# Performance work log

Hardware: AMD Instinct MI355X
Metric: run time of the kernel (lower is better)

The kernel has to match this reference:

```python
import jax, jax.numpy as jnp
import numpy as np

B, L, D_IN = 4, 2048, 80
D, H, DFF, WIN = 128, 16, 128, 64
DH = D // H
BN_EPS = 1e-5


def sinusoidal_positional_encoding(l, d, dtype):
    # Faithful to source: pos_j = 10000 ** (j / d) (exponent j/d, not 2j/d)
    n = d // 2 + (d % 2 == 1)
    pos_i = jnp.arange(l, dtype=dtype)[:, None]                  # [L,1]
    pos_j = jnp.power(jnp.asarray(10000.0, dtype), jnp.arange(n, dtype=dtype) / d)  # [n]
    ang = pos_i / pos_j                                          # [L,n]
    pos = jnp.stack([jnp.sin(ang), jnp.cos(ang)], axis=-1).reshape(l, -1)
    return pos[:, :d]                                            # [L,D]


def local_window_disallowed_mask(l, win):
    # Source: mask starts as ones (True = disallowed), zeros only strictly
    i = jnp.arange(l)
    diff = jnp.abs(i[:, None] - i[None, :])
    allowed = (diff >= 1) & (diff <= win)
    return ~allowed                                              # [L,L] bool, True = masked


def setup_inputs() -> dict:
    key = jax.random.key(0)
    ks = jax.random.split(key, 17)
    s = 0.05  # weight scale for numerical stability
    return {
        "x": jax.random.normal(ks[0], (B, L, D_IN), jnp.float32),
        "conv_w": jax.random.normal(ks[1], (D, D_IN), jnp.float32) * s,
        "conv_b": jax.random.normal(ks[2], (D,), jnp.float32) * s,
        "bn_g": jax.random.uniform(ks[3], (D,), jnp.float32, 0.5, 1.5),
        "bn_b": jax.random.normal(ks[4], (D,), jnp.float32) * s,
        "bn_rm": jax.random.normal(ks[5], (D,), jnp.float32) * s,
        "bn_rv": jax.random.uniform(ks[6], (D,), jnp.float32, 0.5, 1.5),
        "in_proj_w": jax.random.normal(ks[7], (3 * D, D), jnp.float32) * s,
        "in_proj_b": jax.random.normal(ks[8], (3 * D,), jnp.float32) * s,
        "out_w": jax.random.normal(ks[9], (D, D), jnp.float32) * s,
        "out_b": jax.random.normal(ks[10], (D,), jnp.float32) * s,
        "ff_w1": jax.random.normal(ks[11], (DFF, D), jnp.float32) * s,
        "ff_b1": jax.random.normal(ks[12], (DFF,), jnp.float32) * s,
        "ff_w2": jax.random.normal(ks[13], (D, DFF), jnp.float32) * s,
        "ff_b2": jax.random.normal(ks[14], (D,), jnp.float32) * s,
        "fc_w": jax.random.normal(ks[15], (D_IN, D), jnp.float32) * s,
        "fc_b": jax.random.normal(ks[16], (D_IN,), jnp.float32) * s,
    }


def _forward(x, conv_w, conv_b, bn_g, bn_b, bn_rm, bn_rv,
             in_proj_w, in_proj_b, out_w, out_b,
             ff_w1, ff_b1, ff_w2, ff_b2, fc_w, fc_b):
    b, l, _ = x.shape
    dt = x.dtype
    # Conv1d(kernel=1) + ReLU + BatchNorm1d (eval mode, running stats)
    h = jax.nn.relu(jnp.einsum('bli,oi->blo', x, conv_w) + conv_b)     # [B,L,D]
    h = (h - bn_rm) * (bn_g * jax.lax.rsqrt(bn_rv + BN_EPS)) + bn_b
    # positional encoding
    h = h + sinusoidal_positional_encoding(l, D, dt)
    # MultiheadAttention (torch semantics: joint in_proj, scaled dot, out_proj)
    qkv = jnp.einsum('bld,ed->ble', h, in_proj_w) + in_proj_b          # [B,L,3D]
    q, k, v = jnp.split(qkv, 3, axis=-1)
    q = q.reshape(b, l, H, DH).transpose(0, 2, 1, 3)                   # [B,H,L,dh]
    k = k.reshape(b, l, H, DH).transpose(0, 2, 1, 3)
    v = v.reshape(b, l, H, DH).transpose(0, 2, 1, 3)
    scores = jnp.einsum('bhqd,bhkd->bhqk', q, k) / jnp.sqrt(jnp.asarray(DH, dt))
    mask = local_window_disallowed_mask(l, WIN)                        # True = masked
    scores = jnp.where(mask, jnp.finfo(dt).min, scores)
    attn = jax.nn.softmax(scores, axis=-1)                             # [B,H,L,L]
    ctx = jnp.einsum('bhqk,bhkd->bhqd', attn, v)
    ctx = ctx.transpose(0, 2, 1, 3).reshape(b, l, D)
    attn_out = jnp.einsum('bld,od->blo', ctx, out_w) + out_b           # [B,L,D]
    # FFN (no residual in source)
    f = jax.nn.relu(jnp.einsum('bld,fd->blf', attn_out, ff_w1) + ff_b1)
    f = jnp.einsum('blf,df->bld', f, ff_w2) + ff_b2                    # [B,L,D]
    # final head
    return jnp.einsum('bld,od->blo', f, fc_w) + fc_b                   # [B,L,80]


def reference(x, conv_w, conv_b, bn_g, bn_b, bn_rm, bn_rv,
              in_proj_w, in_proj_b, out_w, out_b,
              ff_w1, ff_b1, ff_w2, ff_b2, fc_w, fc_b):
    return _forward(x, conv_w, conv_b, bn_g, bn_b, bn_rm, bn_rv,
                    in_proj_w, in_proj_b, out_w, out_b,
                    ff_w1, ff_b1, ff_w2, ff_b2, fc_w, fc_b)
```

## Files before the change

### kernel.cpp

```cpp
#include <hip/hip_runtime.h>
#include <hip/hip_bf16.h>
#include <math.h>

constexpr int B_ = 4, L_ = 2048, DIN = 80, D_ = 128, H_ = 16, DH = 8;
constexpr int T_ = B_ * L_;
constexpr int LDX = T_;
constexpr int BHL = B_ * H_ * L_;

__device__ float g_xT  [DIN * T_];
__device__ float g_posT[D_ * L_];
__device__ float g_h   [D_ * T_];
__device__ float g_qkv [3 * D_ * T_];
__device__ float g_ctx [D_ * T_];
__device__ float g_f1  [D_ * T_];
__device__ float g_pA  [2 * 8 * BHL];
__device__ float g_pl  [2 * BHL];
__device__ float g_WconvT[DIN * D_];
__device__ float g_WqkvT [D_ * 3 * D_];
__device__ float g_Wf1T  [D_ * D_];
__device__ float g_WfcT  [D_ * D_];
__device__ float g_bf1   [D_];
__device__ float g_bfc   [D_];

__global__ __launch_bounds__(256) void prep_kernel(
        const float* __restrict__ x,
        const float* __restrict__ conv_w,
        const float* __restrict__ in_proj_w,
        const float* __restrict__ out_w,  const float* __restrict__ out_b,
        const float* __restrict__ ff_w1,  const float* __restrict__ ff_b1,
        const float* __restrict__ ff_w2,  const float* __restrict__ ff_b2,
        const float* __restrict__ fc_w,   const float* __restrict__ fc_b) {
    __shared__ float smem[80 * 65];
    int bid = blockIdx.x, tid = threadIdx.x;

    if (bid < 128) {
        int t0 = bid * 64;
        for (int i = tid; i < 64 * 80; i += 256) {
            int t = i / 80, k = i - t * 80;
            smem[k * 65 + t] = x[(size_t)(t0) * 80 + i];
        }
        __syncthreads();
        for (int i = tid; i < 80 * 64; i += 256) {
            int k = i >> 6, tt = i & 63;
            g_xT[(size_t)k * T_ + t0 + tt] = smem[k * 65 + tt];
        }
        return;
    }
    if (bid < 640) {
        int idx = (bid - 128) * 256 + tid;
        int l = idx >> 6, j = idx & 63;
        float inv = __expf((float)j * (-9.210340371976184f / 128.0f));
        float ang = (float)l * inv;
        g_posT[(2 * j) * L_ + l]     = sinf(ang);
        g_posT[(2 * j + 1) * L_ + l] = cosf(ang);
        return;
    }
    if (bid < 680) {
        int e = (bid - 640) * 256 + tid;
        int o = e / 80, k = e - o * 80;
        g_WconvT[k * D_ + o] = conv_w[e];
        return;
    }
    if (bid < 872) {
        int e = (bid - 680) * 256 + tid;
        int o = e >> 7, k = e & 127;
        g_WqkvT[k * (3 * D_) + o] = in_proj_w[e];
        return;
    }
    float* rowbuf = smem;
    float* red = smem + 256;
    if (bid < 936) {
        int sub = tid >> 7, k = tid & 127;
        int f = (bid - 872) * 2 + sub;
        rowbuf[sub * 128 + k] = ff_w1[f * 128 + k];
        __syncthreads();
        float acc = 0.f;
#pragma unroll 8
        for (int o = 0; o < 128; o++)
            acc = fmaf(rowbuf[sub * 128 + o], out_w[o * 128 + k], acc);
        g_Wf1T[k * 128 + f] = acc;
        red[tid] = rowbuf[sub * 128 + k] * out_b[k];
        __syncthreads();
        for (int s = 64; s > 0; s >>= 1) {
            if (k < s) red[tid] += red[tid + s];
            __syncthreads();
        }
        if (k == 0) g_bf1[f] = red[sub * 128] + ff_b1[f];
        return;
    }
    {
        int sub = tid >> 7, k = tid & 127;
        int o = (bid - 936) * 2 + sub;
        rowbuf[sub * 128 + k] = (o < 80) ? fc_w[o * 128 + k] : 0.f;
        __syncthreads();
        float acc = 0.f;
#pragma unroll 8
        for (int d = 0; d < 128; d++)
            acc = fmaf(rowbuf[sub * 128 + d], ff_w2[d * 128 + k], acc);
        g_WfcT[k * 128 + o] = acc;
        red[tid] = rowbuf[sub * 128 + k] * ff_b2[k];
        __syncthreads();
        for (int s = 64; s > 0; s >>= 1) {
            if (k < s) red[tid] += red[tid + s];
            __syncthreads();
        }
        if (k == 0) g_bfc[o] = (o < 80) ? (red[sub * 128] + fc_b[o]) : 0.f;
        return;
    }
}

template <int K, int BK, int BN, int LDW, int EPI>
__global__ __launch_bounds__(256) void gemm_kernel(
        const float* __restrict__ X, const float* __restrict__ Wt,
        const float* __restrict__ bias,
        const float* __restrict__ bg, const float* __restrict__ bb,
        const float* __restrict__ brm, const float* __restrict__ brv,
        float* __restrict__ Y) {
    constexpr int TN = BN / 16;
    __shared__ float Xs[BK][64];
    __shared__ float Ws[BK][BN];
    int tid = threadIdx.x;
    int t0 = blockIdx.x * 64;
    int cb = blockIdx.y * BN;
    int tc = tid & 15, tr = tid >> 4;

    float acc[4][TN] = {};
    for (int kc = 0; kc < K; kc += BK) {
        for (int i = tid; i < BK * 16; i += 256) {
            int k = i >> 4, f = i & 15;
            *(float4*)&Xs[k][f * 4] =
                *(const float4*)&X[(size_t)(kc + k) * LDX + t0 + f * 4];
        }
        for (int i = tid; i < BK * (BN / 4); i += 256) {
            int k = i / (BN / 4), f = i - k * (BN / 4);
            *(float4*)&Ws[k][f * 4] =
                *(const float4*)&Wt[(size_t)(kc + k) * LDW + cb + f * 4];
        }
        __syncthreads();
#pragma unroll 4
        for (int k = 0; k < BK; ++k) {
            float4 a = *(float4*)&Xs[k][tr * 4];
            float av[4] = {a.x, a.y, a.z, a.w};
            float wv[TN];
#pragma unroll
            for (int jj = 0; jj < TN; jj++) wv[jj] = Ws[k][tc * TN + jj];
#pragma unroll
            for (int i = 0; i < 4; i++)
#pragma unroll
                for (int jj = 0; jj < TN; jj++)
                    acc[i][jj] = fmaf(av[i], wv[jj], acc[i][jj]);
        }
        __syncthreads();
    }

    if (EPI == 4) {
#pragma unroll
        for (int jj = 0; jj < TN; jj++) {
            int c = cb + tc * TN + jj;
            if (c < 80) {
                float bv = bias[c];
#pragma unroll
                for (int i = 0; i < 4; i++) {
                    int t = t0 + tr * 4 + i;
                    Y[(size_t)t * 80 + c] = acc[i][jj] + bv;
                }
            }
        }
        return;
    }
#pragma unroll
    for (int jj = 0; jj < TN; jj++) {
        int c = cb + tc * TN + jj;
        float bv = bias[c];
        float vs[4];
#pragma unroll
        for (int i = 0; i < 4; i++) {
            float v = acc[i][jj] + bv;
            if (EPI == 1) v = fmaxf(v, 0.0f);
            if (EPI == 2) {
                v = fmaxf(v, 0.0f);
                v = (v - brm[c]) * (bg[c] * rsqrtf(brv[c] + 1e-5f)) + bb[c];
                v += g_posT[c * L_ + ((t0 & 2047) + tr * 4 + i)];
            }
            vs[i] = v;
        }
        *(float4*)&Y[(size_t)c * LDX + t0 + tr * 4] = *(float4*)vs;
    }
}

__global__ __launch_bounds__(128) void attn_kernel() {
    __shared__ float4 SK[2][2][160];
    __shared__ float4 SV[2][2][160];
    int bh = blockIdx.x, tile = blockIdx.y, hf = blockIdx.z;
    int b = bh >> 4, h = bh & 15;
    int qb = tile * 256;
    int tid = threadIdx.x;
    int jbase = hf ? (qb + 1) : (qb - 64);
    int tb = b * L_;

    for (int c16 = 0; c16 < 16; c16++) {
        int d = (c16 < 8) ? c16 : (c16 - 8);
        int ch = ((c16 < 8) ? 128 : 256) + h * 8 + d;
        const float* src = g_qkv + (size_t)ch * LDX + tb;
        for (int s = tid; s < 319; s += 128) {
            int j = jbase + s;
            float v = ((unsigned)j < (unsigned)L_) ? src[j] : 0.f;
            float4* arr = (c16 < 8) ? &SK[s & 1][d >> 2][s >> 1]
                                    : &SV[s & 1][d >> 2][s >> 1];
            ((float*)arr)[d & 3] = v;
        }
    }
    __syncthreads();

    const float sc = 0.35355339059327373f;
    int q0 = qb + 2 * tid;
    float qa[8], qc[8];
    {
        const float* qsrc = g_qkv + tb;
#pragma unroll
        for (int d = 0; d < 8; d++) {
            qa[d] = qsrc[(size_t)(h * 8 + d) * LDX + q0] * sc;
            qc[d] = qsrc[(size_t)(h * 8 + d) * LDX + q0 + 1] * sc;
        }
    }

    float l0 = 0.f, l1 = 0.f;
    float A0[8] = {}, A1[8] = {};
    int j00 = jbase + 2 * tid;

    auto step = [&](int it, bool m0, bool m1) {
        int p = it & 1, idx = tid + (it >> 1);
        float4 ka = SK[p][0][idx], kb = SK[p][1][idx];
        float kv[8] = {ka.x, ka.y, ka.z, ka.w, kb.x, kb.y, kb.z, kb.w};
        float s0 = 0.f, s1 = 0.f;
#pragma unroll
        for (int d = 0; d < 8; d++) {
            s0 = fmaf(qa[d], kv[d], s0);
            s1 = fmaf(qc[d], kv[d], s1);
        }
        bool jv = (unsigned)(j00 + it) < (unsigned)L_;
        float w0 = (m0 && jv) ? __expf(s0) : 0.f;
        float w1 = (m1 && jv) ? __expf(s1) : 0.f;
        l0 += w0; l1 += w1;
        float4 va = SV[p][0][idx], vb = SV[p][1][idx];
        float vv[8] = {va.x, va.y, va.z, va.w, vb.x, vb.y, vb.z, vb.w};
#pragma unroll
        for (int d = 0; d < 8; d++) {
            A0[d] = fmaf(w0, vv[d], A0[d]);
            A1[d] = fmaf(w1, vv[d], A1[d]);
        }
    };

    step(0, true, false);
#pragma unroll 2
    for (int it = 1; it <= 63; it++) step(it, true, true);
    step(64, false, true);

    int base = bh * L_ + q0;
#pragma unroll
    for (int d = 0; d < 8; d++) {
        g_pA[(hf * 8 + d) * BHL + base]     = A0[d];
        g_pA[(hf * 8 + d) * BHL + base + 1] = A1[d];
    }
    g_pl[hf * BHL + base]     = l0;
    g_pl[hf * BHL + base + 1] = l1;
}

__global__ __launch_bounds__(256) void combine_kernel() {
    int gq = blockIdx.x * 256 + threadIdx.x;
    int bh = gq >> 11, l = gq & 2047;
    int b = bh >> 4, h = bh & 15;
    float ls = g_pl[gq] + g_pl[BHL + gq];
    float inv = 1.f / ls;
#pragma unroll
    for (int d = 0; d < 8; d++) {
        float v = (g_pA[d * BHL + gq] + g_pA[(8 + d) * BHL + gq]) * inv;
        g_ctx[(size_t)(h * 8 + d) * LDX + b * L_ + l] = v;
    }
}

extern "C" void kernel_launch(void* const* d_in, const int* in_sizes, int n_in,
                              void* d_out, int out_size, void* d_ws, size_t ws_size,
                              hipStream_t stream) {
    const float* x         = (const float*)d_in[0];
    const float* conv_w    = (const float*)d_in[1];
    const float* conv_b    = (const float*)d_in[2];
    const float* bn_g      = (const float*)d_in[3];
    const float* bn_b      = (const float*)d_in[4];
    const float* bn_rm     = (const float*)d_in[5];
    const float* bn_rv     = (const float*)d_in[6];
    const float* in_proj_w = (const float*)d_in[7];
    const float* in_proj_b = (const float*)d_in[8];
    const float* out_w     = (const float*)d_in[9];
    const float* out_b     = (const float*)d_in[10];
    const float* ff_w1     = (const float*)d_in[11];
    const float* ff_b1     = (const float*)d_in[12];
    const float* ff_w2     = (const float*)d_in[13];
    const float* ff_b2     = (const float*)d_in[14];
    const float* fc_w      = (const float*)d_in[15];
    const float* fc_b      = (const float*)d_in[16];

    float *p_xT, *p_h, *p_qkv, *p_ctx, *p_f1;
    float *p_WconvT, *p_WqkvT, *p_Wf1T, *p_WfcT, *p_bf1, *p_bfc;
    hipGetSymbolAddress((void**)&p_xT,     HIP_SYMBOL(g_xT));
    hipGetSymbolAddress((void**)&p_h,      HIP_SYMBOL(g_h));
    hipGetSymbolAddress((void**)&p_qkv,    HIP_SYMBOL(g_qkv));
    hipGetSymbolAddress((void**)&p_ctx,    HIP_SYMBOL(g_ctx));
    hipGetSymbolAddress((void**)&p_f1,     HIP_SYMBOL(g_f1));
    hipGetSymbolAddress((void**)&p_WconvT, HIP_SYMBOL(g_WconvT));
    hipGetSymbolAddress((void**)&p_WqkvT,  HIP_SYMBOL(g_WqkvT));
    hipGetSymbolAddress((void**)&p_Wf1T,   HIP_SYMBOL(g_Wf1T));
    hipGetSymbolAddress((void**)&p_WfcT,   HIP_SYMBOL(g_WfcT));
    hipGetSymbolAddress((void**)&p_bf1,    HIP_SYMBOL(g_bf1));
    hipGetSymbolAddress((void**)&p_bfc,    HIP_SYMBOL(g_bfc));

    prep_kernel<<<1000, 256, 0, stream>>>(x, conv_w, in_proj_w, out_w, out_b,
                                          ff_w1, ff_b1, ff_w2, ff_b2, fc_w, fc_b);

    gemm_kernel<80, 80, 32, 128, 2><<<dim3(128, 4), 256, 0, stream>>>(
        p_xT, p_WconvT, conv_b, bn_g, bn_b, bn_rm, bn_rv, p_h);

    gemm_kernel<128, 64, 64, 384, 0><<<dim3(128, 6), 256, 0, stream>>>(
        p_h, p_WqkvT, in_proj_b, nullptr, nullptr, nullptr, nullptr, p_qkv);

    attn_kernel<<<dim3(64, 8, 2), 128, 0, stream>>>();
    combine_kernel<<<512, 256, 0, stream>>>();

    gemm_kernel<128, 128, 32, 128, 1><<<dim3(128, 4), 256, 0, stream>>>(
        p_ctx, p_Wf1T, p_bf1, nullptr, nullptr, nullptr, nullptr, p_f1);

    gemm_kernel<128, 128, 32, 128, 4><<<dim3(128, 3), 256, 0, stream>>>(
        p_f1, p_WfcT, p_bfc, nullptr, nullptr, nullptr, nullptr, (float*)d_out);
}
```

Measured before the change: 164.4 us.

## Merge all stages into one cooperative persistent kernel with grid syncs

```diff
diff --git a/kernel.cpp b/kernel.cpp
--- a/kernel.cpp
+++ b/kernel.cpp
@@ -1,6 +1,8 @@
 #include <hip/hip_runtime.h>
-#include <hip/hip_bf16.h>
+#include <hip/hip_cooperative_groups.h>
 #include <math.h>
+
+namespace cg = cooperative_groups;
 
 constexpr int B_ = 4, L_ = 2048, DIN = 80, D_ = 128, H_ = 16, DH = 8;
 constexpr int T_ = B_ * L_;
@@ -22,192 +24,176 @@
 __device__ float g_bf1   [D_];
 __device__ float g_bfc   [D_];
 
-__global__ __launch_bounds__(256) void prep_kernel(
-        const float* __restrict__ x,
-        const float* __restrict__ conv_w,
-        const float* __restrict__ in_proj_w,
-        const float* __restrict__ out_w,  const float* __restrict__ out_b,
-        const float* __restrict__ ff_w1,  const float* __restrict__ ff_b1,
-        const float* __restrict__ ff_w2,  const float* __restrict__ ff_b2,
-        const float* __restrict__ fc_w,   const float* __restrict__ fc_b) {
-    __shared__ float smem[80 * 65];
-    int bid = blockIdx.x, tid = threadIdx.x;
-
-    if (bid < 128) {
-        int t0 = bid * 64;
+struct Params {
+    const float *x, *conv_w, *conv_b, *bn_g, *bn_b, *bn_rm, *bn_rv;
+    const float *in_proj_w, *in_proj_b, *out_w, *out_b;
+    const float *ff_w1, *ff_b1, *ff_w2, *ff_b2, *fc_w, *fc_b;
+    float* out;
+};
+
+__device__ void prep_unit(int u, int tid, const Params& p, float* smem) {
+    if (u < 128) {
+        int t0 = u * 64;
         for (int i = tid; i < 64 * 80; i += 256) {
             int t = i / 80, k = i - t * 80;
-            smem[k * 65 + t] = x[(size_t)(t0) * 80 + i];
+            smem[k * 65 + t] = p.x[(size_t)t0 * 80 + i];
         }
         __syncthreads();
         for (int i = tid; i < 80 * 64; i += 256) {
             int k = i >> 6, tt = i & 63;
             g_xT[(size_t)k * T_ + t0 + tt] = smem[k * 65 + tt];
         }
-        return;
-    }
-    if (bid < 640) {
-        int idx = (bid - 128) * 256 + tid;
+    } else if (u < 640) {
+        int idx = (u - 128) * 256 + tid;
         int l = idx >> 6, j = idx & 63;
         float inv = __expf((float)j * (-9.210340371976184f / 128.0f));
         float ang = (float)l * inv;
         g_posT[(2 * j) * L_ + l]     = sinf(ang);
         g_posT[(2 * j + 1) * L_ + l] = cosf(ang);
-        return;
-    }
-    if (bid < 680) {
-        int e = (bid - 640) * 256 + tid;
+    } else if (u < 680) {
+        int e = (u - 640) * 256 + tid;
         int o = e / 80, k = e - o * 80;
-        g_WconvT[k * D_ + o] = conv_w[e];
-        return;
-    }
-    if (bid < 872) {
-        int e = (bid - 680) * 256 + tid;
+        g_WconvT[k * D_ + o] = p.conv_w[e];
+    } else if (u < 872) {
+        int e = (u - 680) * 256 + tid;
         int o = e >> 7, k = e & 127;
-        g_WqkvT[k * (3 * D_) + o] = in_proj_w[e];
-        return;
-    }
-    float* rowbuf = smem;
-    float* red = smem + 256;
-    if (bid < 936) {
+        g_WqkvT[k * (3 * D_) + o] = p.in_proj_w[e];
+    } else if (u < 936) {
+        float* rowbuf = smem; float* red = smem + 256;
         int sub = tid >> 7, k = tid & 127;
-        int f = (bid - 872) * 2 + sub;
-        rowbuf[sub * 128 + k] = ff_w1[f * 128 + k];
+        int f = (u - 872) * 2 + sub;
+        rowbuf[sub * 128 + k] = p.ff_w1[f * 128 + k];
         __syncthreads();
         float acc = 0.f;
 #pragma unroll 8
         for (int o = 0; o < 128; o++)
-            acc = fmaf(rowbuf[sub * 128 + o], out_w[o * 128 + k], acc);
+            acc = fmaf(rowbuf[sub * 128 + o], p.out_w[o * 128 + k], acc);
         g_Wf1T[k * 128 + f] = acc;
-        red[tid] = rowbuf[sub * 128 + k] * out_b[k];
+        red[tid] = rowbuf[sub * 128 + k] * p.out_b[k];
         __syncthreads();
         for (int s = 64; s > 0; s >>= 1) {
             if (k < s) red[tid] += red[tid + s];
             __syncthreads();
         }
-        if (k == 0) g_bf1[f] = red[sub * 128] + ff_b1[f];
-        return;
-    }
-    {
+        if (k == 0) g_bf1[f] = red[sub * 128] + p.ff_b1[f];
+    } else {
+        float* rowbuf = smem; float* red = smem + 256;
         int sub = tid >> 7, k = tid & 127;
-        int o = (bid - 936) * 2 + sub;
-        rowbuf[sub * 128 + k] = (o < 80) ? fc_w[o * 128 + k] : 0.f;
+        int o = (u - 936) * 2 + sub;
+        rowbuf[sub * 128 + k] = (o < 80) ? p.fc_w[o * 128 + k] : 0.f;
         __syncthreads();
         float acc = 0.f;
 #pragma unroll 8
         for (int d = 0; d < 128; d++)
-            acc = fmaf(rowbuf[sub * 128 + d], ff_w2[d * 128 + k], acc);
+            acc = fmaf(rowbuf[sub * 128 + d], p.ff_w2[d * 128 + k], acc);
         g_WfcT[k * 128 + o] = acc;
-        red[tid] = rowbuf[sub * 128 + k] * ff_b2[k];
+        red[tid] = rowbuf[sub * 128 + k] * p.ff_b2[k];
         __syncthreads();
         for (int s = 64; s > 0; s >>= 1) {
             if (k < s) red[tid] += red[tid + s];
             __syncthreads();
         }
-        if (k == 0) g_bfc[o] = (o < 80) ? (red[sub * 128] + fc_b[o]) : 0.f;
-        return;
+        if (k == 0) g_bfc[o] = (o < 80) ? (red[sub * 128] + p.fc_b[o]) : 0.f;
     }
 }
 
 template <int K, int BK, int BN, int LDW, int EPI>
-__global__ __launch_bounds__(256) void gemm_kernel(
-        const float* __restrict__ X, const float* __restrict__ Wt,
-        const float* __restrict__ bias,
-        const float* __restrict__ bg, const float* __restrict__ bb,
-        const float* __restrict__ brm, const float* __restrict__ brv,
-        float* __restrict__ Y) {
+__device__ void gemm_tile(float* smem, const float* __restrict__ X,
+                          const float* __restrict__ Wt,
+                          const float* __restrict__ bias,
+                          const float* __restrict__ bg, const float* __restrict__ bb,
+                          const float* __restrict__ brm, const float* __restrict__ brv,
+                          float* __restrict__ Y, int tx, int cy, int tid) {
     constexpr int TN = BN / 16;
-    __shared__ float Xs[BK][64];
-    __shared__ float Ws[BK][BN];
-    int tid = threadIdx.x;
-    int t0 = blockIdx.x * 64;
-    int cb = blockIdx.y * BN;
+    float* Xs = smem;
+    float* Ws = smem + BK * 64;
+    int t0 = tx * 64, cb = cy * BN;
     int tc = tid & 15, tr = tid >> 4;
-
     float acc[4][TN] = {};
     for (int kc = 0; kc < K; kc += BK) {
         for (int i = tid; i < BK * 16; i += 256) {
             int k = i >> 4, f = i & 15;
-            *(float4*)&Xs[k][f * 4] =
+            *(float4*)&Xs[k * 64 + f * 4] =
                 *(const float4*)&X[(size_t)(kc + k) * LDX + t0 + f * 4];
         }
         for (int i = tid; i < BK * (BN / 4); i += 256) {
             int k = i / (BN / 4), f = i - k * (BN / 4);
-            *(float4*)&Ws[k][f * 4] =
+            *(float4*)&Ws[k * BN + f * 4] =
                 *(const float4*)&Wt[(size_t)(kc + k) * LDW + cb + f * 4];
         }
         __syncthreads();
 #pragma unroll 4
         for (int k = 0; k < BK; ++k) {
-            float4 a = *(float4*)&Xs[k][tr * 4];
+            float4 a = *(float4*)&Xs[k * 64 + tr * 4];
             float av[4] = {a.x, a.y, a.z, a.w};
             float wv[TN];
-#pragma unroll
-            for (int jj = 0; jj < TN; jj++) wv[jj] = Ws[k][tc * TN + jj];
+            if (TN == 4) {
+                float4 w = *(float4*)&Ws[k * BN + tc * 4];
+                wv[0] = w.x; wv[1] = w.y; wv[2] = w.z; wv[3] = w.w;
+            } else {
+#pragma unroll
+                for (int j = 0; j < TN; j++) wv[j] = Ws[k * BN + tc * TN + j];
+            }
 #pragma unroll
             for (int i = 0; i < 4; i++)
 #pragma unroll
-                for (int jj = 0; jj < TN; jj++)
-                    acc[i][jj] = fmaf(av[i], wv[jj], acc[i][jj]);
-        }
-        __syncthreads();
-    }
-
+                for (int j = 0; j < TN; j++)
+                    acc[i][j] = fmaf(av[i], wv[j], acc[i][j]);
+        }
+        __syncthreads();
+    }
     if (EPI == 4) {
 #pragma unroll
-        for (int jj = 0; jj < TN; jj++) {
-            int c = cb + tc * TN + jj;
+        for (int j = 0; j < TN; j++) {
+            int c = cb + tc * TN + j;
             if (c < 80) {
                 float bv = bias[c];
 #pragma unroll
-                for (int i = 0; i < 4; i++) {
-                    int t = t0 + tr * 4 + i;
-                    Y[(size_t)t * 80 + c] = acc[i][jj] + bv;
+                for (int i = 0; i < 4; i++)
+                    Y[(size_t)(t0 + tr * 4 + i) * 80 + c] = acc[i][j] + bv;
+            }
+        }
+    } else {
+#pragma unroll
+        for (int j = 0; j < TN; j++) {
+            int c = cb + tc * TN + j;
+            float bv = bias[c];
+            float vs[4];
+#pragma unroll
+            for (int i = 0; i < 4; i++) {
+                float v = acc[i][j] + bv;
+                if (EPI == 1) v = fmaxf(v, 0.0f);
+                if (EPI == 2) {
+                    v = fmaxf(v, 0.0f);
+                    v = (v - brm[c]) * (bg[c] * rsqrtf(brv[c] + 1e-5f)) + bb[c];
+                    v += g_posT[c * L_ + ((t0 & 2047) + tr * 4 + i)];
                 }
+                vs[i] = v;
             }
-        }
-        return;
-    }
-#pragma unroll
-    for (int jj = 0; jj < TN; jj++) {
-        int c = cb + tc * TN + jj;
-        float bv = bias[c];
-        float vs[4];
-#pragma unroll
-        for (int i = 0; i < 4; i++) {
-            float v = acc[i][jj] + bv;
-            if (EPI == 1) v = fmaxf(v, 0.0f);
-            if (EPI == 2) {
-                v = fmaxf(v, 0.0f);
-                v = (v - brm[c]) * (bg[c] * rsqrtf(brv[c] + 1e-5f)) + bb[c];
-                v += g_posT[c * L_ + ((t0 & 2047) + tr * 4 + i)];
-            }
-            vs[i] = v;
-        }
-        *(float4*)&Y[(size_t)c * LDX + t0 + tr * 4] = *(float4*)vs;
-    }
-}
-
-__global__ __launch_bounds__(128) void attn_kernel() {
-    __shared__ float4 SK[2][2][160];
-    __shared__ float4 SV[2][2][160];
-    int bh = blockIdx.x, tile = blockIdx.y, hf = blockIdx.z;
+            *(float4*)&Y[(size_t)c * LDX + t0 + tr * 4] = *(float4*)vs;
+        }
+    }
+}
+
+__device__ void attn_stage(float* smem, int bid, int tid) {
+    int bh = bid >> 3, sub = bid & 7;
+    int qt = sub >> 1, hf = sub & 1;
+    int qb = qt * 512;
     int b = bh >> 4, h = bh & 15;
-    int qb = tile * 256;
-    int tid = threadIdx.x;
+    int tb = b * L_;
     int jbase = hf ? (qb + 1) : (qb - 64);
-    int tb = b * L_;
+    float4* SK = (float4*)smem;
+    float4* SV = SK + 1152;
 
     for (int c16 = 0; c16 < 16; c16++) {
-        int d = (c16 < 8) ? c16 : (c16 - 8);
-        int ch = ((c16 < 8) ? 128 : 256) + h * 8 + d;
+        int d = c16 & 7;
+        int ch = ((c16 < 8) ? D_ : 2 * D_) + h * 8 + d;
         const float* src = g_qkv + (size_t)ch * LDX + tb;
-        for (int s = tid; s < 319; s += 128) {
+        float4* base4 = ((c16 < 8) ? SK : SV) + (d >> 2) * 288;
+        for (int s = tid; s < 575; s += 256) {
             int j = jbase + s;
             float v = ((unsigned)j < (unsigned)L_) ? src[j] : 0.f;
-            float4* arr = (c16 < 8) ? &SK[s & 1][d >> 2][s >> 1]
-                                    : &SV[s & 1][d >> 2][s >> 1];
-            ((float*)arr)[d & 3] = v;
+            ((float*)(base4 + (s & 1) * 576 + (s >> 1)))[d & 3] = v;
         }
     }
     __syncthreads();
@@ -215,23 +201,20 @@
     const float sc = 0.35355339059327373f;
     int q0 = qb + 2 * tid;
     float qa[8], qc[8];
-    {
-        const float* qsrc = g_qkv + tb;
-#pragma unroll
-        for (int d = 0; d < 8; d++) {
-            qa[d] = qsrc[(size_t)(h * 8 + d) * LDX + q0] * sc;
-            qc[d] = qsrc[(size_t)(h * 8 + d) * LDX + q0 + 1] * sc;
-        }
-    }
-
+#pragma unroll
+    for (int d = 0; d < 8; d++) {
+        qa[d] = g_qkv[(size_t)(h * 8 + d) * LDX + tb + q0] * sc;
+        qc[d] = g_qkv[(size_t)(h * 8 + d) * LDX + tb + q0 + 1] * sc;
+    }
     float l0 = 0.f, l1 = 0.f;
     float A0[8] = {}, A1[8] = {};
     int j00 = jbase + 2 * tid;
 
-    auto step = [&](int it, bool m0, bool m1) {
-        int p = it & 1, idx = tid + (it >> 1);
-        float4 ka = SK[p][0][idx], kb = SK[p][1][idx];
-        float kv[8] = {ka.x, ka.y, ka.z, ka.w, kb.x, kb.y, kb.z, kb.w};
+#pragma unroll 1
+    for (int it = 0; it <= 64; it++) {
+        int pp = it & 1, idx = tid + (it >> 1);
+        float4 ka = SK[pp * 576 + idx], kb2 = SK[pp * 576 + 288 + idx];
+        float kv[8] = {ka.x, ka.y, ka.z, ka.w, kb2.x, kb2.y, kb2.z, kb2.w};
         float s0 = 0.f, s1 = 0.f;
 #pragma unroll
         for (int d = 0; d < 8; d++) {
@@ -239,96 +222,103 @@
             s1 = fmaf(qc[d], kv[d], s1);
         }
         bool jv = (unsigned)(j00 + it) < (unsigned)L_;
-        float w0 = (m0 && jv) ? __expf(s0) : 0.f;
-        float w1 = (m1 && jv) ? __expf(s1) : 0.f;
+        float w0 = (jv && it <= 63) ? __expf(s0) : 0.f;
+        float w1 = (jv && it >= 1)  ? __expf(s1) : 0.f;
         l0 += w0; l1 += w1;
-        float4 va = SV[p][0][idx], vb = SV[p][1][idx];
-        float vv[8] = {va.x, va.y, va.z, va.w, vb.x, vb.y, vb.z, vb.w};
+        float4 va = SV[pp * 576 + idx], vb2 = SV[pp * 576 + 288 + idx];
+        float vv[8] = {va.x, va.y, va.z, va.w, vb2.x, vb2.y, vb2.z, vb2.w};
 #pragma unroll
         for (int d = 0; d < 8; d++) {
             A0[d] = fmaf(w0, vv[d], A0[d]);
             A1[d] = fmaf(w1, vv[d], A1[d]);
         }
-    };
-
-    step(0, true, false);
-#pragma unroll 2
-    for (int it = 1; it <= 63; it++) step(it, true, true);
-    step(64, false, true);
-
+    }
     int base = bh * L_ + q0;
 #pragma unroll
     for (int d = 0; d < 8; d++) {
-        g_pA[(hf * 8 + d) * BHL + base]     = A0[d];
-        g_pA[(hf * 8 + d) * BHL + base + 1] = A1[d];
+        g_pA[(size_t)(hf * 8 + d) * BHL + base]     = A0[d];
+        g_pA[(size_t)(hf * 8 + d) * BHL + base + 1] = A1[d];
     }
     g_pl[hf * BHL + base]     = l0;
     g_pl[hf * BHL + base + 1] = l1;
 }
 
-__global__ __launch_bounds__(256) void combine_kernel() {
-    int gq = blockIdx.x * 256 + threadIdx.x;
+__device__ void combine_unit(int bid, int tid) {
+    int gq = bid * 256 + tid;
     int bh = gq >> 11, l = gq & 2047;
     int b = bh >> 4, h = bh & 15;
-    float ls = g_pl[gq] + g_pl[BHL + gq];
-    float inv = 1.f / ls;
+    float inv = 1.f / (g_pl[gq] + g_pl[BHL + gq]);
 #pragma unroll
     for (int d = 0; d < 8; d++) {
-        float v = (g_pA[d * BHL + gq] + g_pA[(8 + d) * BHL + gq]) * inv;
+        float v = (g_pA[(size_t)d * BHL + gq] + g_pA[(size_t)(8 + d) * BHL + gq]) * inv;
         g_ctx[(size_t)(h * 8 + d) * LDX + b * L_ + l] = v;
     }
+}
+
+__global__ __launch_bounds__(256, 2) void mega_kernel(Params p) {
+    cg::grid_group grid = cg::this_grid();
+    __shared__ float smem[9216];
+    int bid = blockIdx.x, tid = threadIdx.x;
+
+    for (int u = bid; u < 1000; u += 512) {
+        prep_unit(u, tid, p, smem);
+        __syncthreads();
+    }
+    grid.sync();
+
+    gemm_tile<80, 80, 32, 128, 2>(smem, g_xT, g_WconvT, p.conv_b,
+                                  p.bn_g, p.bn_b, p.bn_rm, p.bn_rv,
+                                  g_h, bid & 127, bid >> 7, tid);
+    grid.sync();
+
+    for (int u = bid; u < 768; u += 512)
+        gemm_tile<128, 64, 64, 384, 0>(smem, g_h, g_WqkvT, p.in_proj_b,
+                                       nullptr, nullptr, nullptr, nullptr,
+                                       g_qkv, u & 127, u >> 7, tid);
+    grid.sync();
+
+    attn_stage(smem, bid, tid);
+    grid.sync();
+
+    combine_unit(bid, tid);
+    grid.sync();
+
+    if (bid < 256)
+        gemm_tile<128, 64, 64, 128, 1>(smem, g_ctx, g_Wf1T, g_bf1,
+                                       nullptr, nullptr, nullptr, nullptr,
+                                       g_f1, bid & 127, bid >> 7, tid);
+    grid.sync();
+
+    if (bid < 256)
+        gemm_tile<128, 64, 64, 128, 4>(smem, g_f1, g_WfcT, g_bfc,
+                                       nullptr, nullptr, nullptr, nullptr,
+                                       p.out, bid & 127, bid >> 7, tid);
 }
 
 extern "C" void kernel_launch(void* const* d_in, const int* in_sizes, int n_in,
                               void* d_out, int out_size, void* d_ws, size_t ws_size,
                               hipStream_t stream) {
-    const float* x         = (const float*)d_in[0];
-    const float* conv_w    = (const float*)d_in[1];
-    const float* conv_b    = (const float*)d_in[2];
-    const float* bn_g      = (const float*)d_in[3];
-    const float* bn_b      = (const float*)d_in[4];
-    const float* bn_rm     = (const float*)d_in[5];
-    const float* bn_rv     = (const float*)d_in[6];
-    const float* in_proj_w = (const float*)d_in[7];
-    const float* in_proj_b = (const float*)d_in[8];
-    const float* out_w     = (const float*)d_in[9];
-    const float* out_b     = (const float*)d_in[10];
-    const float* ff_w1     = (const float*)d_in[11];
-    const float* ff_b1     = (const float*)d_in[12];
-    const float* ff_w2     = (const float*)d_in[13];
-    const float* ff_b2     = (const float*)d_in[14];
-    const float* fc_w      = (const float*)d_in[15];
-    const float* fc_b      = (const float*)d_in[16];
-
-    float *p_xT, *p_h, *p_qkv, *p_ctx, *p_f1;
-    float *p_WconvT, *p_WqkvT, *p_Wf1T, *p_WfcT, *p_bf1, *p_bfc;
-    hipGetSymbolAddress((void**)&p_xT,     HIP_SYMBOL(g_xT));
-    hipGetSymbolAddress((void**)&p_h,      HIP_SYMBOL(g_h));
-    hipGetSymbolAddress((void**)&p_qkv,    HIP_SYMBOL(g_qkv));
-    hipGetSymbolAddress((void**)&p_ctx,    HIP_SYMBOL(g_ctx));
-    hipGetSymbolAddress((void**)&p_f1,     HIP_SYMBOL(g_f1));
-    hipGetSymbolAddress((void**)&p_WconvT, HIP_SYMBOL(g_WconvT));
-    hipGetSymbolAddress((void**)&p_WqkvT,  HIP_SYMBOL(g_WqkvT));
-    hipGetSymbolAddress((void**)&p_Wf1T,   HIP_SYMBOL(g_Wf1T));
-    hipGetSymbolAddress((void**)&p_WfcT,   HIP_SYMBOL(g_WfcT));
-    hipGetSymbolAddress((void**)&p_bf1,    HIP_SYMBOL(g_bf1));
-    hipGetSymbolAddress((void**)&p_bfc,    HIP_SYMBOL(g_bfc));
-
-    prep_kernel<<<1000, 256, 0, stream>>>(x, conv_w, in_proj_w, out_w, out_b,
-                                          ff_w1, ff_b1, ff_w2, ff_b2, fc_w, fc_b);
-
-    gemm_kernel<80, 80, 32, 128, 2><<<dim3(128, 4), 256, 0, stream>>>(
-        p_xT, p_WconvT, conv_b, bn_g, bn_b, bn_rm, bn_rv, p_h);
-
-    gemm_kernel<128, 64, 64, 384, 0><<<dim3(128, 6), 256, 0, stream>>>(
-        p_h, p_WqkvT, in_proj_b, nullptr, nullptr, nullptr, nullptr, p_qkv);
-
-    attn_kernel<<<dim3(64, 8, 2), 128, 0, stream>>>();
-    combine_kernel<<<512, 256, 0, stream>>>();
-
-    gemm_kernel<128, 128, 32, 128, 1><<<dim3(128, 4), 256, 0, stream>>>(
-        p_ctx, p_Wf1T, p_bf1, nullptr, nullptr, nullptr, nullptr, p_f1);
-
-    gemm_kernel<128, 128, 32, 128, 4><<<dim3(128, 3), 256, 0, stream>>>(
-        p_f1, p_WfcT, p_bfc, nullptr, nullptr, nullptr, nullptr, (float*)d_out);
-}
+    Params hp;
+    hp.x         = (const float*)d_in[0];
+    hp.conv_w    = (const float*)d_in[1];
+    hp.conv_b    = (const float*)d_in[2];
+    hp.bn_g      = (const float*)d_in[3];
+    hp.bn_b      = (const float*)d_in[4];
+    hp.bn_rm     = (const float*)d_in[5];
+    hp.bn_rv     = (const float*)d_in[6];
+    hp.in_proj_w = (const float*)d_in[7];
+    hp.in_proj_b = (const float*)d_in[8];
+    hp.out_w     = (const float*)d_in[9];
+    hp.out_b     = (const float*)d_in[10];
+    hp.ff_w1     = (const float*)d_in[11];
+    hp.ff_b1     = (const float*)d_in[12];
+    hp.ff_w2     = (const float*)d_in[13];
+    hp.ff_b2     = (const float*)d_in[14];
+    hp.fc_w      = (const float*)d_in[15];
+    hp.fc_b      = (const float*)d_in[16];
+    hp.out       = (float*)d_out;
+
+    void* kargs[] = {(void*)&hp};
+    hipLaunchCooperativeKernel((const void*)mega_kernel, dim3(512), dim3(256),
+                               kargs, 0, stream);
+}
```

New measurement: 562.2 us. 242% more time.

## Fuse attention halves and combine into single-pass windowed attention kernel

Applied to the files above, without the earlier changes.

```diff
diff --git a/kernel.cpp b/kernel.cpp
--- a/kernel.cpp
+++ b/kernel.cpp
@@ -1,11 +1,9 @@
 #include <hip/hip_runtime.h>
-#include <hip/hip_bf16.h>
 #include <math.h>
 
 constexpr int B_ = 4, L_ = 2048, DIN = 80, D_ = 128, H_ = 16, DH = 8;
 constexpr int T_ = B_ * L_;
 constexpr int LDX = T_;
-constexpr int BHL = B_ * H_ * L_;
 
 __device__ float g_xT  [DIN * T_];
 __device__ float g_posT[D_ * L_];
@@ -13,8 +11,6 @@
 __device__ float g_qkv [3 * D_ * T_];
 __device__ float g_ctx [D_ * T_];
 __device__ float g_f1  [D_ * T_];
-__device__ float g_pA  [2 * 8 * BHL];
-__device__ float g_pl  [2 * BHL];
 __device__ float g_WconvT[DIN * D_];
 __device__ float g_WqkvT [D_ * 3 * D_];
 __device__ float g_Wf1T  [D_ * D_];
@@ -37,7 +33,7 @@
         int t0 = bid * 64;
         for (int i = tid; i < 64 * 80; i += 256) {
             int t = i / 80, k = i - t * 80;
-            smem[k * 65 + t] = x[(size_t)(t0) * 80 + i];
+            smem[k * 65 + t] = x[(size_t)t0 * 80 + i];
         }
         __syncthreads();
         for (int i = tid; i < 80 * 64; i += 256) {
@@ -188,26 +184,25 @@
     }
 }
 
-__global__ __launch_bounds__(128) void attn_kernel() {
-    __shared__ float4 SK[2][2][160];
-    __shared__ float4 SV[2][2][160];
-    int bh = blockIdx.x, tile = blockIdx.y, hf = blockIdx.z;
+__global__ __launch_bounds__(256) void attn_kernel() {
+    __shared__ float4 SK[2][2][324];
+    __shared__ float4 SV[2][2][324];
+    int bh = blockIdx.x;
+    int qb = blockIdx.y * 512;
     int b = bh >> 4, h = bh & 15;
-    int qb = tile * 256;
+    int tb = b * L_;
     int tid = threadIdx.x;
-    int jbase = hf ? (qb + 1) : (qb - 64);
-    int tb = b * L_;
+    int jbase = qb - 64;
 
     for (int c16 = 0; c16 < 16; c16++) {
-        int d = (c16 < 8) ? c16 : (c16 - 8);
-        int ch = ((c16 < 8) ? 128 : 256) + h * 8 + d;
+        int d = c16 & 7;
+        int ch = ((c16 < 8) ? D_ : 2 * D_) + h * 8 + d;
         const float* src = g_qkv + (size_t)ch * LDX + tb;
-        for (int s = tid; s < 319; s += 128) {
+        float4* base4 = ((c16 < 8) ? &SK[0][0][0] : &SV[0][0][0]) + (d >> 2) * 324;
+        for (int s = tid; s < 641; s += 256) {
             int j = jbase + s;
             float v = ((unsigned)j < (unsigned)L_) ? src[j] : 0.f;
-            float4* arr = (c16 < 8) ? &SK[s & 1][d >> 2][s >> 1]
-                                    : &SV[s & 1][d >> 2][s >> 1];
-            ((float*)arr)[d & 3] = v;
+            ((float*)(base4 + (s & 1) * 648 + (s >> 1)))[d & 3] = v;
         }
     }
     __syncthreads();
@@ -215,23 +210,20 @@
     const float sc = 0.35355339059327373f;
     int q0 = qb + 2 * tid;
     float qa[8], qc[8];
-    {
-        const float* qsrc = g_qkv + tb;
-#pragma unroll
-        for (int d = 0; d < 8; d++) {
-            qa[d] = qsrc[(size_t)(h * 8 + d) * LDX + q0] * sc;
-            qc[d] = qsrc[(size_t)(h * 8 + d) * LDX + q0 + 1] * sc;
-        }
-    }
-
+#pragma unroll
+    for (int d = 0; d < 8; d++) {
+        qa[d] = g_qkv[(size_t)(h * 8 + d) * LDX + tb + q0] * sc;
+        qc[d] = g_qkv[(size_t)(h * 8 + d) * LDX + tb + q0 + 1] * sc;
+    }
     float l0 = 0.f, l1 = 0.f;
     float A0[8] = {}, A1[8] = {};
     int j00 = jbase + 2 * tid;
 
-    auto step = [&](int it, bool m0, bool m1) {
-        int p = it & 1, idx = tid + (it >> 1);
-        float4 ka = SK[p][0][idx], kb = SK[p][1][idx];
-        float kv[8] = {ka.x, ka.y, ka.z, ka.w, kb.x, kb.y, kb.z, kb.w};
+#pragma unroll 2
+    for (int it = 0; it <= 129; it++) {
+        int pp = it & 1, idx = tid + (it >> 1);
+        float4 ka = SK[pp][0][idx], kb2 = SK[pp][1][idx];
+        float kv[8] = {ka.x, ka.y, ka.z, ka.w, kb2.x, kb2.y, kb2.z, kb2.w};
         float s0 = 0.f, s1 = 0.f;
 #pragma unroll
         for (int d = 0; d < 8; d++) {
@@ -239,43 +231,23 @@
             s1 = fmaf(qc[d], kv[d], s1);
         }
         bool jv = (unsigned)(j00 + it) < (unsigned)L_;
-        float w0 = (m0 && jv) ? __expf(s0) : 0.f;
-        float w1 = (m1 && jv) ? __expf(s1) : 0.f;
+        float w0 = (jv && it != 64 && it <= 128) ? __expf(s0) : 0.f;
+        float w1 = (jv && it != 65 && it >= 1)  ? __expf(s1) : 0.f;
         l0 += w0; l1 += w1;
-        float4 va = SV[p][0][idx], vb = SV[p][1][idx];
-        float vv[8] = {va.x, va.y, va.z, va.w, vb.x, vb.y, vb.z, vb.w};
+        float4 va = SV[pp][0][idx], vb2 = SV[pp][1][idx];
+        float vv[8] = {va.x, va.y, va.z, va.w, vb2.x, vb2.y, vb2.z, vb2.w};
 #pragma unroll
         for (int d = 0; d < 8; d++) {
             A0[d] = fmaf(w0, vv[d], A0[d]);
             A1[d] = fmaf(w1, vv[d], A1[d]);
         }
-    };
-
-    step(0, true, false);
-#pragma unroll 2
-    for (int it = 1; it <= 63; it++) step(it, true, true);
-    step(64, false, true);
-
-    int base = bh * L_ + q0;
+    }
+    float i0 = 1.f / l0, i1 = 1.f / l1;
+    int base = tb + q0;
 #pragma unroll
     for (int d = 0; d < 8; d++) {
-        g_pA[(hf * 8 + d) * BHL + base]     = A0[d];
-        g_pA[(hf * 8 + d) * BHL + base + 1] = A1[d];
-    }
-    g_pl[hf * BHL + base]     = l0;
-    g_pl[hf * BHL + base + 1] = l1;
-}
-
-__global__ __launch_bounds__(256) void combine_kernel() {
-    int gq = blockIdx.x * 256 + threadIdx.x;
-    int bh = gq >> 11, l = gq & 2047;
-    int b = bh >> 4, h = bh & 15;
-    float ls = g_pl[gq] + g_pl[BHL + gq];
-    float inv = 1.f / ls;
-#pragma unroll
-    for (int d = 0; d < 8; d++) {
-        float v = (g_pA[d * BHL + gq] + g_pA[(8 + d) * BHL + gq]) * inv;
-        g_ctx[(size_t)(h * 8 + d) * LDX + b * L_ + l] = v;
+        g_ctx[(size_t)(h * 8 + d) * LDX + base]     = A0[d] * i0;
+        g_ctx[(size_t)(h * 8 + d) * LDX + base + 1] = A1[d] * i1;
     }
 }
 
@@ -323,8 +295,7 @@
     gemm_kernel<128, 64, 64, 384, 0><<<dim3(128, 6), 256, 0, stream>>>(
         p_h, p_WqkvT, in_proj_b, nullptr, nullptr, nullptr, nullptr, p_qkv);
 
-    attn_kernel<<<dim3(64, 8, 2), 128, 0, stream>>>();
-    combine_kernel<<<512, 256, 0, stream>>>();
+    attn_kernel<<<dim3(64, 4), 256, 0, stream>>>();
 
     gemm_kernel<128, 128, 32, 128, 1><<<dim3(128, 4), 256, 0, stream>>>(
         p_ctx, p_Wf1T, p_bf1, nullptr, nullptr, nullptr, nullptr, p_f1);
```

Result: no change. 167.6 us (+2.0%).

## Compute QKV projection with split-bf16 MFMA and token-major hi/lo activations

Applied to the files above, without the earlier changes.

```diff
diff --git a/kernel.cpp b/kernel.cpp
--- a/kernel.cpp
+++ b/kernel.cpp
@@ -1,26 +1,39 @@
 #include <hip/hip_runtime.h>
-#include <hip/hip_bf16.h>
 #include <math.h>
 
-constexpr int B_ = 4, L_ = 2048, DIN = 80, D_ = 128, H_ = 16, DH = 8;
-constexpr int T_ = B_ * L_;
+constexpr int L_ = 2048, D_ = 128, H_ = 16;
+constexpr int T_ = 8192;
+constexpr int DIN = 80;
 constexpr int LDX = T_;
-constexpr int BHL = B_ * H_ * L_;
+constexpr int BHL = 131072;
+
+typedef __attribute__((ext_vector_type(8))) short short8;
+typedef __attribute__((ext_vector_type(4))) float floatx4;
 
 __device__ float g_xT  [DIN * T_];
 __device__ float g_posT[D_ * L_];
-__device__ float g_h   [D_ * T_];
+__device__ unsigned short g_h_hi[T_ * D_];
+__device__ unsigned short g_h_lo[T_ * D_];
+__device__ unsigned short g_Wq_hi[3 * D_ * D_];
+__device__ unsigned short g_Wq_lo[3 * D_ * D_];
 __device__ float g_qkv [3 * D_ * T_];
 __device__ float g_ctx [D_ * T_];
 __device__ float g_f1  [D_ * T_];
 __device__ float g_pA  [2 * 8 * BHL];
 __device__ float g_pl  [2 * BHL];
 __device__ float g_WconvT[DIN * D_];
-__device__ float g_WqkvT [D_ * 3 * D_];
 __device__ float g_Wf1T  [D_ * D_];
 __device__ float g_WfcT  [D_ * D_];
 __device__ float g_bf1   [D_];
 __device__ float g_bfc   [D_];
+
+__device__ __forceinline__ unsigned short bf16h(float x) {
+    unsigned u = __float_as_uint(x);
+    return (unsigned short)((u + 0x7FFFu + ((u >> 16) & 1u)) >> 16);
+}
+__device__ __forceinline__ float bf16f(unsigned short h) {
+    return __uint_as_float(((unsigned)h) << 16);
+}
 
 __global__ __launch_bounds__(256) void prep_kernel(
         const float* __restrict__ x,
@@ -37,7 +50,7 @@
         int t0 = bid * 64;
         for (int i = tid; i < 64 * 80; i += 256) {
             int t = i / 80, k = i - t * 80;
-            smem[k * 65 + t] = x[(size_t)(t0) * 80 + i];
+            smem[k * 65 + t] = x[(size_t)t0 * 80 + i];
         }
         __syncthreads();
         for (int i = tid; i < 80 * 64; i += 256) {
@@ -63,8 +76,10 @@
     }
     if (bid < 872) {
         int e = (bid - 680) * 256 + tid;
-        int o = e >> 7, k = e & 127;
-        g_WqkvT[k * (3 * D_) + o] = in_proj_w[e];
+        float v = in_proj_w[e];
+        unsigned short hi = bf16h(v);
+        g_Wq_hi[e] = hi;
+        g_Wq_lo[e] = bf16h(v - bf16f(hi));
         return;
     }
     float* rowbuf = smem;
@@ -153,6 +168,29 @@
         __syncthreads();
     }
 
+    if (EPI == 5) {
+#pragma unroll
+        for (int i = 0; i < 4; i++) {
+            int t = t0 + tr * 4 + i;
+            unsigned hi2 = 0, lo2 = 0;
+#pragma unroll
+            for (int jj = 0; jj < TN; jj++) {
+                int c = cb + tc * TN + jj;
+                float v = acc[i][jj] + bias[c];
+                v = fmaxf(v, 0.0f);
+                v = (v - brm[c]) * (bg[c] * rsqrtf(brv[c] + 1e-5f)) + bb[c];
+                v += g_posT[c * L_ + (t & 2047)];
+                unsigned short h = bf16h(v);
+                float lo = v - bf16f(h);
+                hi2 |= ((unsigned)h) << (16 * jj);
+                lo2 |= ((unsigned)bf16h(lo)) << (16 * jj);
+            }
+            int cbase = cb + tc * TN;
+            *(unsigned*)&g_h_hi[(size_t)t * 128 + cbase] = hi2;
+            *(unsigned*)&g_h_lo[(size_t)t * 128 + cbase] = lo2;
+        }
+        return;
+    }
     if (EPI == 4) {
 #pragma unroll
         for (int jj = 0; jj < TN; jj++) {
@@ -177,14 +215,63 @@
         for (int i = 0; i < 4; i++) {
             float v = acc[i][jj] + bv;
             if (EPI == 1) v = fmaxf(v, 0.0f);
-            if (EPI == 2) {
-                v = fmaxf(v, 0.0f);
-                v = (v - brm[c]) * (bg[c] * rsqrtf(brv[c] + 1e-5f)) + bb[c];
-                v += g_posT[c * L_ + ((t0 & 2047) + tr * 4 + i)];
-            }
             vs[i] = v;
         }
         *(float4*)&Y[(size_t)c * LDX + t0 + tr * 4] = *(float4*)vs;
+    }
+}
+
+__global__ __launch_bounds__(256) void qkv_mfma(const float* __restrict__ in_proj_b) {
+    __shared__ unsigned short WsH[64 * 136];
+    __shared__ unsigned short WsL[64 * 136];
+    __shared__ unsigned short HsH[32 * 136];
+    __shared__ unsigned short HsL[32 * 136];
+    int tid = threadIdx.x;
+    int t0 = blockIdx.x * 32;
+    int cb = blockIdx.y * 64;
+
+    for (int i = tid; i < 1024; i += 256) {
+        int r = i >> 4, c8 = (i & 15) * 8;
+        *(uint4*)&WsH[r * 136 + c8] = *(const uint4*)&g_Wq_hi[(size_t)(cb + r) * 128 + c8];
+        *(uint4*)&WsL[r * 136 + c8] = *(const uint4*)&g_Wq_lo[(size_t)(cb + r) * 128 + c8];
+    }
+    for (int i = tid; i < 512; i += 256) {
+        int r = i >> 4, c8 = (i & 15) * 8;
+        *(uint4*)&HsH[r * 136 + c8] = *(const uint4*)&g_h_hi[(size_t)(t0 + r) * 128 + c8];
+        *(uint4*)&HsL[r * 136 + c8] = *(const uint4*)&g_h_lo[(size_t)(t0 + r) * 128 + c8];
+    }
+    __syncthreads();
+
+    int lane = tid & 63, w = tid >> 6;
+    int m16 = lane & 15, quad = lane >> 4;
+    int c0 = w * 16;
+
+    short8 aH[4], aL[4];
+#pragma unroll
+    for (int kt = 0; kt < 4; kt++) {
+        aH[kt] = *(short8*)&WsH[(c0 + m16) * 136 + kt * 32 + quad * 8];
+        aL[kt] = *(short8*)&WsL[(c0 + m16) * 136 + kt * 32 + quad * 8];
+    }
+    float bias_r[4];
+#pragma unroll
+    for (int r = 0; r < 4; r++) bias_r[r] = in_proj_b[cb + c0 + quad * 4 + r];
+
+#pragma unroll
+    for (int s = 0; s < 2; s++) {
+        floatx4 acc = {0.f, 0.f, 0.f, 0.f};
+        int trow = s * 16 + m16;
+#pragma unroll
+        for (int kt = 0; kt < 4; kt++) {
+            short8 bH = *(short8*)&HsH[trow * 136 + kt * 32 + quad * 8];
+            short8 bL = *(short8*)&HsL[trow * 136 + kt * 32 + quad * 8];
+            acc = __builtin_amdgcn_mfma_f32_16x16x32_bf16(aH[kt], bH, acc, 0, 0, 0);
+            acc = __builtin_amdgcn_mfma_f32_16x16x32_bf16(aL[kt], bH, acc, 0, 0, 0);
+            acc = __builtin_amdgcn_mfma_f32_16x16x32_bf16(aH[kt], bL, acc, 0, 0, 0);
+        }
+#pragma unroll
+        for (int r = 0; r < 4; r++)
+            g_qkv[(size_t)(cb + c0 + quad * 4 + r) * LDX + t0 + s * 16 + m16] =
+                acc[r] + bias_r[r];
     }
 }
 
@@ -199,8 +286,8 @@
     int tb = b * L_;
 
     for (int c16 = 0; c16 < 16; c16++) {
-        int d = (c16 < 8) ? c16 : (c16 - 8);
-        int ch = ((c16 < 8) ? 128 : 256) + h * 8 + d;
+        int d = c16 & 7;
+        int ch = ((c16 < 8) ? D_ : 2 * D_) + h * 8 + d;
         const float* src = g_qkv + (size_t)ch * LDX + tb;
         for (int s = tid; s < 319; s += 128) {
             int j = jbase + s;
@@ -215,13 +302,10 @@
     const float sc = 0.35355339059327373f;
     int q0 = qb + 2 * tid;
     float qa[8], qc[8];
-    {
-        const float* qsrc = g_qkv + tb;
-#pragma unroll
-        for (int d = 0; d < 8; d++) {
-            qa[d] = qsrc[(size_t)(h * 8 + d) * LDX + q0] * sc;
-            qc[d] = qsrc[(size_t)(h * 8 + d) * LDX + q0 + 1] * sc;
-        }
+#pragma unroll
+    for (int d = 0; d < 8; d++) {
+        qa[d] = g_qkv[(size_t)(h * 8 + d) * LDX + tb + q0] * sc;
+        qc[d] = g_qkv[(size_t)(h * 8 + d) * LDX + tb + q0 + 1] * sc;
     }
 
     float l0 = 0.f, l1 = 0.f;
@@ -259,8 +343,8 @@
     int base = bh * L_ + q0;
 #pragma unroll
     for (int d = 0; d < 8; d++) {
-        g_pA[(hf * 8 + d) * BHL + base]     = A0[d];
-        g_pA[(hf * 8 + d) * BHL + base + 1] = A1[d];
+        g_pA[(size_t)(hf * 8 + d) * BHL + base]     = A0[d];
+        g_pA[(size_t)(hf * 8 + d) * BHL + base + 1] = A1[d];
     }
     g_pl[hf * BHL + base]     = l0;
     g_pl[hf * BHL + base + 1] = l1;
@@ -270,11 +354,10 @@
     int gq = blockIdx.x * 256 + threadIdx.x;
     int bh = gq >> 11, l = gq & 2047;
     int b = bh >> 4, h = bh & 15;
-    float ls = g_pl[gq] + g_pl[BHL + gq];
-    float inv = 1.f / ls;
+    float inv = 1.f / (g_pl[gq] + g_pl[BHL + gq]);
 #pragma unroll
     for (int d = 0; d < 8; d++) {
-        float v = (g_pA[d * BHL + gq] + g_pA[(8 + d) * BHL + gq]) * inv;
+        float v = (g_pA[(size_t)d * BHL + gq] + g_pA[(size_t)(8 + d) * BHL + gq]) * inv;
         g_ctx[(size_t)(h * 8 + d) * LDX + b * L_ + l] = v;
     }
 }
@@ -300,15 +383,11 @@
     const float* fc_w      = (const float*)d_in[15];
     const float* fc_b      = (const float*)d_in[16];
 
-    float *p_xT, *p_h, *p_qkv, *p_ctx, *p_f1;
-    float *p_WconvT, *p_WqkvT, *p_Wf1T, *p_WfcT, *p_bf1, *p_bfc;
+    float *p_xT, *p_WconvT, *p_ctx, *p_f1, *p_Wf1T, *p_WfcT, *p_bf1, *p_bfc;
     hipGetSymbolAddress((void**)&p_xT,     HIP_SYMBOL(g_xT));
-    hipGetSymbolAddress((void**)&p_h,      HIP_SYMBOL(g_h));
-    hipGetSymbolAddress((void**)&p_qkv,    HIP_SYMBOL(g_qkv));
+    hipGetSymbolAddress((void**)&p_WconvT, HIP_SYMBOL(g_WconvT));
     hipGetSymbolAddress((void**)&p_ctx,    HIP_SYMBOL(g_ctx));
     hipGetSymbolAddress((void**)&p_f1,     HIP_SYMBOL(g_f1));
-    hipGetSymbolAddress((void**)&p_WconvT, HIP_SYMBOL(g_WconvT));
-    hipGetSymbolAddress((void**)&p_WqkvT,  HIP_SYMBOL(g_WqkvT));
     hipGetSymbolAddress((void**)&p_Wf1T,   HIP_SYMBOL(g_Wf1T));
     hipGetSymbolAddress((void**)&p_WfcT,   HIP_SYMBOL(g_WfcT));
     hipGetSymbolAddress((void**)&p_bf1,    HIP_SYMBOL(g_bf1));
@@ -317,11 +396,10 @@
     prep_kernel<<<1000, 256, 0, stream>>>(x, conv_w, in_proj_w, out_w, out_b,
                                           ff_w1, ff_b1, ff_w2, ff_b2, fc_w, fc_b);
 
-    gemm_kernel<80, 80, 32, 128, 2><<<dim3(128, 4), 256, 0, stream>>>(
-        p_xT, p_WconvT, conv_b, bn_g, bn_b, bn_rm, bn_rv, p_h);
-
-    gemm_kernel<128, 64, 64, 384, 0><<<dim3(128, 6), 256, 0, stream>>>(
-        p_h, p_WqkvT, in_proj_b, nullptr, nullptr, nullptr, nullptr, p_qkv);
+    gemm_kernel<80, 80, 32, 128, 5><<<dim3(128, 4), 256, 0, stream>>>(
+        p_xT, p_WconvT, conv_b, bn_g, bn_b, bn_rm, bn_rv, nullptr);
+
+    qkv_mfma<<<dim3(256, 6), 256, 0, stream>>>(in_proj_b);
 
     attn_kernel<<<dim3(64, 8, 2), 128, 0, stream>>>();
     combine_kernel<<<512, 256, 0, stream>>>();
```

New measurement: 163.2 us. No clear change (-0.7%).
